# Kernel tuning notes

Measured on AMD Instinct MI355X. Metric: run time of the kernel, lower is better.

## Reference

```python
import jax, jax.numpy as jnp
import numpy as np

B, S, D, H = 8, 2048, 1024, 1024

def setup_inputs() -> dict:
    key = jax.random.key(0)
    ks = jax.random.split(key, 7)
    s = 1.0 / np.sqrt(D)  # torch Linear default init scale (uniform bound)
    x = jax.random.normal(ks[0], (B, S, D), dtype=jnp.float32)
    Wq = jax.random.uniform(ks[1], (D, H), jnp.float32, -s, s)
    bq = jax.random.uniform(ks[2], (H,), jnp.float32, -s, s)
    Wk = jax.random.uniform(ks[3], (D, H), jnp.float32, -s, s)
    bk = jax.random.uniform(ks[4], (H,), jnp.float32, -s, s)
    Wv = jax.random.uniform(ks[5], (D, H), jnp.float32, -s, s)
    bv = jax.random.uniform(ks[6], (H,), jnp.float32, -s, s)
    return {"x": x, "Wq": Wq, "bq": bq, "Wk": Wk, "bk": bk, "Wv": Wv, "bv": bv}

def reference(x, Wq, bq, Wk, bk, Wv, bv):
    scale = jnp.asarray(H ** 0.5, x.dtype)
    q = jnp.einsum('bsd,dh->bsh', x, Wq) + bq
    k = jnp.einsum('bsd,dh->bsh', x, Wk) + bk
    v = jnp.einsum('bsd,dh->bsh', x, Wv) + bv
    scores = jnp.einsum('bqh,bkh->bqk', q, k) / scale  # [B,S,S]
    probs = jax.nn.softmax(scores, axis=-1)
    return jnp.einsum('bqk,bkh->bqh', probs, v)
```

## Files before the change

kernel.cpp:

```cpp
#include <hip/hip_runtime.h>
#include <hip/hip_bf16.h>
#include <stdint.h>

using bf16 = __hip_bfloat16;
typedef __bf16 bf16x8 __attribute__((ext_vector_type(8)));
typedef float f32x4 __attribute__((ext_vector_type(4)));
typedef unsigned short u16x8 __attribute__((ext_vector_type(8)));

#define GLOAD_LDS16(gp, lp)                                                    \
  __builtin_amdgcn_global_load_lds(                                           \
      (const __attribute__((address_space(1))) void*)(gp),                     \
      (__attribute__((address_space(3))) void*)(lp), 16, 0, 0)

#define WAITCNT_VM(N) asm volatile("s_waitcnt vmcnt(" #N ")" ::: "memory")
#define WAITCNT_LGKM0() asm volatile("s_waitcnt lgkmcnt(0)" ::: "memory")

__device__ inline void store_out(bf16* p, float v)  { *p = __float2bfloat16(v); }
__device__ inline void store_out(float* p, float v) { *p = v; }

template <typename OUT_T, int BIAS_AXIS, bool NFAST>
__global__ __launch_bounds__(512, 2) void gemm256(
    const bf16* __restrict__ A, const bf16* __restrict__ Bt,
    const float* __restrict__ bias0, const float* __restrict__ bias1,
    OUT_T* __restrict__ out0, OUT_T* __restrict__ out1, int Nsplit,
    int K, int lda, int ldb, int ldc,
    long long sA, long long sB, long long sC, float alpha)
{
    __shared__ __align__(16) bf16 lds[4 * 16384];

    const int Mt = gridDim.x, Nt = gridDim.y;
    const int nwg = Mt * Nt * gridDim.z;
    const int hw  = blockIdx.x + Mt * (blockIdx.y + Nt * blockIdx.z);
    const int lg  = (nwg & 7) ? hw : ((hw & 7) * (nwg >> 3) + (hw >> 3));
    const int per = Mt * Nt;
    const int zt  = lg / per;
    const int rem = lg - zt * per;
    int mt, nt;
    if (NFAST) { mt = rem / Nt; nt = rem - mt * Nt; }
    else       { mt = rem % Mt; nt = rem / Mt; }

    A  += (long long)zt * sA;
    Bt += (long long)zt * sB;
    out0 += (long long)zt * sC;
    if (out1) out1 += (long long)zt * sC;

    const int bm = mt * 256;
    const int bn = nt * 256;
    const int t = threadIdx.x, lane = t & 63, w = t >> 6;
    const int wm = w >> 2, wn = w & 3;
    const int fr = lane & 15, c16 = lane >> 4;

    const bf16* gsrc[4];
    int lbase[4];
    #pragma unroll
    for (int c = 0; c < 4; ++c) {
        const int idx  = w * 128 + (c & 1) * 64 + lane;
        const int slot = idx & 7;
        const int r    = ((idx >> 3) << 1) | (idx & 1);
        const int cc   = (slot ^ (r & 7)) >> 1;
        if (c < 2) {
            gsrc[c]  = A + (long long)(bm + r) * lda + cc * 8;
            lbase[c] = w * 1024 + c * 512;
        } else {
            gsrc[c]  = Bt + (long long)(bn + r) * ldb + cc * 8;
            lbase[c] = 8192 + w * 1024 + (c - 2) * 512;
        }
    }

    const int sw   = ((fr & 7) ^ (c16 << 1)) * 8;
    const int offA = (wm * 64 + (fr >> 1)) * 64 + sw;
    const int offB = 8192 + (wn * 32 + (fr >> 1)) * 64 + sw;

    const int nk = K >> 5;

    auto STAGE2 = [&](int jt, int h) {
        const int buf = (jt & 3) * 16384;
        GLOAD_LDS16(gsrc[2 * h]     + jt * 32, &lds[buf + lbase[2 * h]]);
        GLOAD_LDS16(gsrc[2 * h + 1] + jt * 32, &lds[buf + lbase[2 * h + 1]]);
    };

    STAGE2(0, 0); STAGE2(0, 1);
    STAGE2(1, 0); STAGE2(1, 1);
    STAGE2(2, 0); STAGE2(2, 1);
    WAITCNT_VM(8);
    __builtin_amdgcn_s_barrier();

    f32x4 acc[8][4] = {};

    for (int j = 0; j < nk; ++j) {
        const int buf = (j & 3) * 16384;
        const bool pref = (j + 3 < nk);

        bf16x8 af[4], bfv[4], af2[4];
        #pragma unroll
        for (int m = 0; m < 4; ++m)
            af[m] = *reinterpret_cast<const bf16x8*>(&lds[buf + offA + m * 512]);
        #pragma unroll
        for (int n = 0; n < 4; ++n)
            bfv[n] = *reinterpret_cast<const bf16x8*>(&lds[buf + offB + n * 512]);
        if (pref) STAGE2(j + 3, 0);

        __builtin_amdgcn_s_barrier();
        WAITCNT_LGKM0();
        __builtin_amdgcn_sched_barrier(0);
        __builtin_amdgcn_s_setprio(1);
        #pragma unroll
        for (int m = 0; m < 4; ++m)
            #pragma unroll
            for (int n = 0; n < 4; ++n)
                acc[m][n] = __builtin_amdgcn_mfma_f32_16x16x32_bf16(
                    af[m], bfv[n], acc[m][n], 0, 0, 0);
        __builtin_amdgcn_s_setprio(0);
        __builtin_amdgcn_sched_barrier(0);
        __builtin_amdgcn_s_barrier();

        #pragma unroll
        for (int m = 0; m < 4; ++m)
            af2[m] = *reinterpret_cast<const bf16x8*>(
                &lds[buf + offA + (m + 4) * 512]);
        if (pref) STAGE2(j + 3, 1);

        __builtin_amdgcn_s_barrier();
        WAITCNT_LGKM0();
        __builtin_amdgcn_sched_barrier(0);
        __builtin_amdgcn_s_setprio(1);
        #pragma unroll
        for (int m = 0; m < 4; ++m)
            #pragma unroll
            for (int n = 0; n < 4; ++n)
                acc[m + 4][n] = __builtin_amdgcn_mfma_f32_16x16x32_bf16(
                    af2[m], bfv[n], acc[m + 4][n], 0, 0, 0);
        __builtin_amdgcn_s_setprio(0);
        __builtin_amdgcn_sched_barrier(0);

        if (j + 3 < nk)      { WAITCNT_VM(8); }
        else if (j + 2 < nk) { WAITCNT_VM(4); }
        else if (j + 1 < nk) { WAITCNT_VM(0); }
        __builtin_amdgcn_s_barrier();
    }

    const int colbase = bn + wn * 64 + fr;
    const int rowbase = bm + wm * 128 + c16 * 4;
    #pragma unroll
    for (int n = 0; n < 4; ++n) {
        const int gc = colbase + n * 16;
        const bool seg0 = gc < Nsplit;
        OUT_T* op = seg0 ? out0 : out1;
        const int col = seg0 ? gc : gc - Nsplit;
        float bcol = 0.0f;
        if (BIAS_AXIS == 0) {
            const float* bp = seg0 ? bias0 : bias1;
            if (bp) bcol = bp[col];
        }
        #pragma unroll
        for (int m = 0; m < 8; ++m) {
            #pragma unroll
            for (int jj = 0; jj < 4; ++jj) {
                const int row = rowbase + m * 16 + jj;
                float v = acc[m][n][jj] * alpha;
                if (BIAS_AXIS == 0) v += bcol;
                else if (bias0)     v += bias0[row];
                store_out(&op[(long long)row * ldc + col], v);
            }
        }
    }
}

__global__ __launch_bounds__(256) void f32_to_bf16(
    const float* __restrict__ in, bf16* __restrict__ out, long long n)
{
    long long i = ((long long)blockIdx.x * 256 + threadIdx.x) * 4;
    const long long stride = (long long)gridDim.x * 256 * 4;
    for (; i < n; i += stride) {
        float4 v = *reinterpret_cast<const float4*>(in + i);
        unsigned ux = __float_as_uint(v.x), uy = __float_as_uint(v.y);
        unsigned uz = __float_as_uint(v.z), uw = __float_as_uint(v.w);
        ushort4 o;
        o.x = (unsigned short)((ux + 0x7fffu + ((ux >> 16) & 1u)) >> 16);
        o.y = (unsigned short)((uy + 0x7fffu + ((uy >> 16) & 1u)) >> 16);
        o.z = (unsigned short)((uz + 0x7fffu + ((uz >> 16) & 1u)) >> 16);
        o.w = (unsigned short)((uw + 0x7fffu + ((uw >> 16) & 1u)) >> 16);
        *reinterpret_cast<ushort4*>(out + i) = o;
    }
}

__global__ void transpose_f32_bf16(const float* __restrict__ in,
                                   bf16* __restrict__ out, int R, int C)
{
    __shared__ float tile[32][33];
    const int c0 = blockIdx.x * 32, r0 = blockIdx.y * 32;
    const int tx = threadIdx.x, ty = threadIdx.y;
    #pragma unroll
    for (int i = ty; i < 32; i += 8)
        tile[i][tx] = in[(long long)(r0 + i) * C + (c0 + tx)];
    __syncthreads();
    #pragma unroll
    for (int i = ty; i < 32; i += 8)
        out[(long long)(c0 + i) * R + (r0 + tx)] = __float2bfloat16(tile[tx][i]);
}

__global__ __launch_bounds__(256) void softmax_rows(bf16* __restrict__ Sbuf, int cols)
{
    __shared__ float red[8];
    bf16* p = Sbuf + (long long)blockIdx.x * cols;
    const int t = threadIdx.x;

    u16x8 v = *reinterpret_cast<const u16x8*>(p + t * 8);
    float f[8];
    #pragma unroll
    for (int i = 0; i < 8; ++i)
        f[i] = __uint_as_float((unsigned)v[i] << 16);

    float m = -3.0e38f;
    #pragma unroll
    for (int i = 0; i < 8; ++i) m = fmaxf(m, f[i]);
    #pragma unroll
    for (int o = 32; o; o >>= 1) m = fmaxf(m, __shfl_xor(m, o));
    if ((t & 63) == 0) red[t >> 6] = m;
    __syncthreads();
    m = fmaxf(fmaxf(red[0], red[1]), fmaxf(red[2], red[3]));

    float s = 0.0f;
    #pragma unroll
    for (int i = 0; i < 8; ++i) { f[i] = __expf(f[i] - m); s += f[i]; }
    #pragma unroll
    for (int o = 32; o; o >>= 1) s += __shfl_xor(s, o);
    __syncthreads();
    if ((t & 63) == 0) red[4 + (t >> 6)] = s;
    __syncthreads();
    s = (red[4] + red[5]) + (red[6] + red[7]);
    const float inv = 1.0f / s;

    u16x8 o16;
    #pragma unroll
    for (int i = 0; i < 8; ++i) {
        unsigned u = __float_as_uint(f[i] * inv);
        o16[i] = (unsigned short)((u + 0x7fffu + ((u >> 16) & 1u)) >> 16);
    }
    *reinterpret_cast<u16x8*>(p + t * 8) = o16;
}

extern "C" void kernel_launch(void* const* d_in, const int* in_sizes, int n_in,
                              void* d_out, int out_size, void* d_ws, size_t ws_size,
                              hipStream_t stream)
{
    const int B = 8, S = 2048, D = 1024, H = 1024;
    const float* x  = (const float*)d_in[0];
    const float* Wq = (const float*)d_in[1];
    const float* bq = (const float*)d_in[2];
    const float* Wk = (const float*)d_in[3];
    const float* bk = (const float*)d_in[4];
    const float* Wv = (const float*)d_in[5];
    const float* bv = (const float*)d_in[6];
    float* out = (float*)d_out;

    const size_t nQKV = (size_t)B * S * H;
    const size_t nW   = (size_t)D * H;
    const long long sSH = (long long)S * H;
    const long long sSS = (long long)S * S;

    dim3 tb(32, 8), g256(256), g512(512);
    const float inv_scale = 1.0f / 32.0f;

    bf16* xb   = (bf16*)d_ws;
    bf16* Q    = xb  + nQKV;
    bf16* Kb   = Q   + nQKV;
    bf16* Vt   = Kb  + nQKV;
    bf16* WtQK = Vt  + nQKV;
    bf16* Wtv  = WtQK + 2 * nW;
    bf16* Sc   = Wtv + nW;

    const size_t tierA = (4 * nQKV + 3 * nW + (size_t)B * S * S) * 2;
    const size_t tierB = (4 * nQKV + 3 * nW + (size_t)S * S) * 2;
    const bool bigA = ws_size >= tierA;
    if (ws_size < tierB) return;

    f32_to_bf16<<<dim3(2048), g256, 0, stream>>>(x, xb, (long long)nQKV);
    transpose_f32_bf16<<<dim3(H / 32, D / 32), tb, 0, stream>>>(Wq, WtQK, D, H);
    transpose_f32_bf16<<<dim3(H / 32, D / 32), tb, 0, stream>>>(Wk, WtQK + nW, D, H);
    transpose_f32_bf16<<<dim3(H / 32, D / 32), tb, 0, stream>>>(Wv, Wtv, D, H);

    gemm256<bf16, 0, true><<<dim3(B * S / 256, 2 * H / 256, 1), g512, 0, stream>>>(
        xb, WtQK, bq, bk, Q, Kb, H, D, D, D, H, 0, 0, 0, 1.0f);

    gemm256<bf16, 1, false><<<dim3(H / 256, B * S / 256, 1), g512, 0, stream>>>(
        Wtv, xb, bv, nullptr, Vt, nullptr, 1 << 30, D, D, D, B * S, 0, 0, 0, 1.0f);

    if (bigA) {
        gemm256<bf16, 0, true><<<dim3(S / 256, S / 256, B), g512, 0, stream>>>(
            Q, Kb, nullptr, nullptr, Sc, nullptr, 1 << 30, H, H, H, S,
            sSH, sSH, sSS, inv_scale);
        softmax_rows<<<dim3(B * S), g256, 0, stream>>>(Sc, S);
        gemm256<float, 0, true><<<dim3(S / 256, H / 256, B), g512, 0, stream>>>(
            Sc, Vt, nullptr, nullptr, out, nullptr, 1 << 30, S, S, B * S, H,
            sSS, (long long)S, sSH, 1.0f);
    } else {
        for (int b = 0; b < B; ++b) {
            gemm256<bf16, 0, true><<<dim3(S / 256, S / 256, 1), g512, 0, stream>>>(
                Q + (size_t)b * sSH, Kb + (size_t)b * sSH, nullptr, nullptr,
                Sc, nullptr, 1 << 30, H, H, H, S, 0, 0, 0, inv_scale);
            softmax_rows<<<dim3(S), g256, 0, stream>>>(Sc, S);
            gemm256<float, 0, true><<<dim3(S / 256, H / 256, 1), g512, 0, stream>>>(
                Sc, Vt + (size_t)b * S, nullptr, nullptr,
                out + (size_t)b * sSH, nullptr, 1 << 30, S, S, B * S, H,
                0, 0, 0, 1.0f);
        }
    }
}
```

Before: 351.6 us.

## Restructure GEMM main loop to K=64 double-buffered quadrant schedule

Rewrites the 256x256 GEMM mainloop so each K-step covers 64 elements instead of 32, with two LDS buffers instead of four. Each K-step is split into four quadrant MFMA phases, and global-to-LDS loads for the next tile are interleaved between them, in the style of a ping-pong schedule. The change aims to raise the MFMA work done per barrier and per LDS read, and to hide load latency better. In exchange it adds more barriers, and it assumes K is a multiple of 128, which risks breaking if K does not divide evenly.

```diff
diff --git a/kernel.cpp b/kernel.cpp
--- a/kernel.cpp
+++ b/kernel.cpp
@@ -12,11 +12,31 @@
       (const __attribute__((address_space(1))) void*)(gp),                     \
       (__attribute__((address_space(3))) void*)(lp), 16, 0, 0)
 
-#define WAITCNT_VM(N) asm volatile("s_waitcnt vmcnt(" #N ")" ::: "memory")
+#define WAITCNT_VM0() asm volatile("s_waitcnt vmcnt(0)" ::: "memory")
+#define WAITCNT_VM2() asm volatile("s_waitcnt vmcnt(2)" ::: "memory")
 #define WAITCNT_LGKM0() asm volatile("s_waitcnt lgkmcnt(0)" ::: "memory")
+#define CFENCE() asm volatile("" ::: "memory")
+#define BAR() do { CFENCE(); __builtin_amdgcn_s_barrier(); CFENCE(); } while (0)
 
 __device__ inline void store_out(bf16* p, float v)  { *p = __float2bfloat16(v); }
 __device__ inline void store_out(float* p, float v) { *p = v; }
+
+template <int QM, int QN>
+__device__ __forceinline__ void mfma_q(f32x4 (&acc)[8][4],
+                                       const bf16x8 (&AV)[4][2],
+                                       const bf16x8 (&BV)[2][2])
+{
+    #pragma unroll
+    for (int kk = 0; kk < 2; ++kk)
+        #pragma unroll
+        for (int mf = 0; mf < 4; ++mf)
+            #pragma unroll
+            for (int nf = 0; nf < 2; ++nf)
+                acc[QM * 4 + mf][QN * 2 + nf] =
+                    __builtin_amdgcn_mfma_f32_16x16x32_bf16(
+                        AV[mf][kk], BV[nf][kk],
+                        acc[QM * 4 + mf][QN * 2 + nf], 0, 0, 0);
+}
 
 template <typename OUT_T, int BIAS_AXIS, bool NFAST>
 __global__ __launch_bounds__(512, 2) void gemm256(
@@ -26,7 +46,7 @@
     int K, int lda, int ldb, int ldc,
     long long sA, long long sB, long long sC, float alpha)
 {
-    __shared__ __align__(16) bf16 lds[4 * 16384];
+    __shared__ __align__(16) bf16 lds[65536];
 
     const int Mt = gridDim.x, Nt = gridDim.y;
     const int nwg = Mt * Nt * gridDim.z;
@@ -35,108 +55,120 @@
     const int per = Mt * Nt;
     const int zt  = lg / per;
     const int rem = lg - zt * per;
-    int mt, nt;
-    if (NFAST) { mt = rem / Nt; nt = rem - mt * Nt; }
-    else       { mt = rem % Mt; nt = rem / Mt; }
+    int mt, ntile;
+    if (NFAST) { mt = rem / Nt; ntile = rem - mt * Nt; }
+    else       { mt = rem % Mt; ntile = rem / Mt; }
 
     A  += (long long)zt * sA;
     Bt += (long long)zt * sB;
     out0 += (long long)zt * sC;
     if (out1) out1 += (long long)zt * sC;
 
-    const int bm = mt * 256;
-    const int bn = nt * 256;
-    const int t = threadIdx.x, lane = t & 63, w = t >> 6;
-    const int wm = w >> 2, wn = w & 3;
+    const int bm = mt * 256, bn = ntile * 256;
+    const int t = threadIdx.x, lane = t & 63;
+    const int w = t >> 6, wm = w >> 2, wn = w & 3;
     const int fr = lane & 15, c16 = lane >> 4;
 
-    const bf16* gsrc[4];
-    int lbase[4];
-    #pragma unroll
-    for (int c = 0; c < 4; ++c) {
-        const int idx  = w * 128 + (c & 1) * 64 + lane;
-        const int slot = idx & 7;
-        const int r    = ((idx >> 3) << 1) | (idx & 1);
-        const int cc   = (slot ^ (r & 7)) >> 1;
-        if (c < 2) {
-            gsrc[c]  = A + (long long)(bm + r) * lda + cc * 8;
-            lbase[c] = w * 1024 + c * 512;
-        } else {
-            gsrc[c]  = Bt + (long long)(bn + r) * ldb + cc * 8;
-            lbase[c] = 8192 + w * 1024 + (c - 2) * 512;
-        }
-    }
-
-    const int sw   = ((fr & 7) ^ (c16 << 1)) * 8;
-    const int offA = (wm * 64 + (fr >> 1)) * 64 + sw;
-    const int offB = 8192 + (wn * 32 + (fr >> 1)) * 64 + sw;
-
-    const int nk = K >> 5;
-
-    auto STAGE2 = [&](int jt, int h) {
-        const int buf = (jt & 3) * 16384;
-        GLOAD_LDS16(gsrc[2 * h]     + jt * 32, &lds[buf + lbase[2 * h]]);
-        GLOAD_LDS16(gsrc[2 * h + 1] + jt * 32, &lds[buf + lbase[2 * h + 1]]);
-    };
-
-    STAGE2(0, 0); STAGE2(0, 1);
-    STAGE2(1, 0); STAGE2(1, 1);
-    STAGE2(2, 0); STAGE2(2, 1);
-    WAITCNT_VM(8);
-    __builtin_amdgcn_s_barrier();
+    const int sr  = t >> 3;
+    const int scc = ((t & 7) ^ (sr & 7)) << 3;
+    const bf16* pA = A  + (long long)(bm + sr) * lda + scc;
+    const bf16* pB = Bt + (long long)(bn + sr) * ldb + scc;
+    const int ldst = t * 8;
+
+#define STAGE_A(HALF, JT, BUFO) do {                                           \
+    const bf16* _s = pA + (long long)(HALF) * 128 * lda + (JT) * 64;           \
+    GLOAD_LDS16(_s, &lds[(BUFO) + (HALF) * 8192 + ldst]);                      \
+    GLOAD_LDS16(_s + 64 * (long long)lda,                                      \
+                &lds[(BUFO) + (HALF) * 8192 + ldst + 4096]);                   \
+} while (0)
+#define STAGE_B(HALF, JT, BUFO) do {                                           \
+    const bf16* _s = pB + (long long)(HALF) * 128 * ldb + (JT) * 64;           \
+    GLOAD_LDS16(_s, &lds[(BUFO) + 16384 + (HALF) * 8192 + ldst]);              \
+    GLOAD_LDS16(_s + 64 * (long long)ldb,                                      \
+                &lds[(BUFO) + 16384 + (HALF) * 8192 + ldst + 4096]);           \
+} while (0)
+
+    const int axor0 = ((c16    ) ^ (fr & 7)) << 3;
+    const int axor1 = ((c16 + 4) ^ (fr & 7)) << 3;
+    const int aoffc = wm * 8192 + fr * 64;
+    const int boffc = 16384 + (wn * 64 + fr) * 64;
+
+#define RD(e) (*reinterpret_cast<const bf16x8*>(&lds[(e)]))
+#define READ_A(QM, BUFO) do {                                                  \
+    _Pragma("unroll") for (int mf = 0; mf < 4; ++mf) {                         \
+        aA[mf][0] = RD((BUFO) + aoffc + (QM) * 4096 + mf * 1024 + axor0);      \
+        aA[mf][1] = RD((BUFO) + aoffc + (QM) * 4096 + mf * 1024 + axor1);      \
+    } } while (0)
+#define READ_B(QN, BV, BUFO) do {                                              \
+    _Pragma("unroll") for (int nf = 0; nf < 2; ++nf) {                         \
+        BV[nf][0] = RD((BUFO) + boffc + (QN) * 2048 + nf * 1024 + axor0);      \
+        BV[nf][1] = RD((BUFO) + boffc + (QN) * 2048 + nf * 1024 + axor1);      \
+    } } while (0)
+
+    const int nk = K >> 6;
+    const int niter = nk >> 1;
 
     f32x4 acc[8][4] = {};
-
-    for (int j = 0; j < nk; ++j) {
-        const int buf = (j & 3) * 16384;
-        const bool pref = (j + 3 < nk);
-
-        bf16x8 af[4], bfv[4], af2[4];
-        #pragma unroll
-        for (int m = 0; m < 4; ++m)
-            af[m] = *reinterpret_cast<const bf16x8*>(&lds[buf + offA + m * 512]);
-        #pragma unroll
-        for (int n = 0; n < 4; ++n)
-            bfv[n] = *reinterpret_cast<const bf16x8*>(&lds[buf + offB + n * 512]);
-        if (pref) STAGE2(j + 3, 0);
-
-        __builtin_amdgcn_s_barrier();
-        WAITCNT_LGKM0();
-        __builtin_amdgcn_sched_barrier(0);
-        __builtin_amdgcn_s_setprio(1);
-        #pragma unroll
-        for (int m = 0; m < 4; ++m)
-            #pragma unroll
-            for (int n = 0; n < 4; ++n)
-                acc[m][n] = __builtin_amdgcn_mfma_f32_16x16x32_bf16(
-                    af[m], bfv[n], acc[m][n], 0, 0, 0);
+    bf16x8 aA[4][2], bQ0[2][2], bQ1[2][2];
+
+    STAGE_A(0, 0, 0); STAGE_A(1, 0, 0); STAGE_B(0, 0, 0); STAGE_B(1, 0, 0);
+    STAGE_A(0, 1, 32768);
+    WAITCNT_VM2();
+    BAR();
+
+    for (int it = 0; it < niter; ++it) {
+        const int t2 = it * 2;
+        const bool tail = (it == niter - 1);
+
+        READ_A(0, 0); READ_B(0, bQ0, 0);
+        STAGE_A(1, t2 + 1, 32768);
+        BAR(); WAITCNT_LGKM0(); __builtin_amdgcn_sched_barrier(0);
+        __builtin_amdgcn_s_setprio(1); mfma_q<0, 0>(acc, aA, bQ0);
+        __builtin_amdgcn_s_setprio(0); BAR();
+
+        READ_B(1, bQ1, 0);
+        STAGE_B(0, t2 + 1, 32768);
+        BAR(); WAITCNT_LGKM0(); __builtin_amdgcn_sched_barrier(0);
+        __builtin_amdgcn_s_setprio(1); mfma_q<0, 1>(acc, aA, bQ1);
+        __builtin_amdgcn_s_setprio(0); BAR();
+
+        READ_A(1, 0);
+        STAGE_B(1, t2 + 1, 32768);
+        BAR(); WAITCNT_LGKM0(); __builtin_amdgcn_sched_barrier(0);
+        __builtin_amdgcn_s_setprio(1); mfma_q<1, 1>(acc, aA, bQ1);
+        __builtin_amdgcn_s_setprio(0); BAR();
+
+        if (!tail) STAGE_A(0, t2 + 2, 0);
+        BAR();
+        __builtin_amdgcn_s_setprio(1); mfma_q<1, 0>(acc, aA, bQ0);
         __builtin_amdgcn_s_setprio(0);
-        __builtin_amdgcn_sched_barrier(0);
-        __builtin_amdgcn_s_barrier();
-
-        #pragma unroll
-        for (int m = 0; m < 4; ++m)
-            af2[m] = *reinterpret_cast<const bf16x8*>(
-                &lds[buf + offA + (m + 4) * 512]);
-        if (pref) STAGE2(j + 3, 1);
-
-        __builtin_amdgcn_s_barrier();
-        WAITCNT_LGKM0();
-        __builtin_amdgcn_sched_barrier(0);
-        __builtin_amdgcn_s_setprio(1);
-        #pragma unroll
-        for (int m = 0; m < 4; ++m)
-            #pragma unroll
-            for (int n = 0; n < 4; ++n)
-                acc[m + 4][n] = __builtin_amdgcn_mfma_f32_16x16x32_bf16(
-                    af2[m], bfv[n], acc[m + 4][n], 0, 0, 0);
+        if (tail) { WAITCNT_VM0(); } else { WAITCNT_VM2(); }
+        BAR();
+
+        READ_A(0, 32768); READ_B(0, bQ0, 32768);
+        if (!tail) STAGE_A(1, t2 + 2, 0);
+        BAR(); WAITCNT_LGKM0(); __builtin_amdgcn_sched_barrier(0);
+        __builtin_amdgcn_s_setprio(1); mfma_q<0, 0>(acc, aA, bQ0);
+        __builtin_amdgcn_s_setprio(0); BAR();
+
+        READ_B(1, bQ1, 32768);
+        if (!tail) STAGE_B(0, t2 + 2, 0);
+        BAR(); WAITCNT_LGKM0(); __builtin_amdgcn_sched_barrier(0);
+        __builtin_amdgcn_s_setprio(1); mfma_q<0, 1>(acc, aA, bQ1);
+        __builtin_amdgcn_s_setprio(0); BAR();
+
+        READ_A(1, 32768);
+        if (!tail) STAGE_B(1, t2 + 2, 0);
+        BAR(); WAITCNT_LGKM0(); __builtin_amdgcn_sched_barrier(0);
+        __builtin_amdgcn_s_setprio(1); mfma_q<1, 1>(acc, aA, bQ1);
+        __builtin_amdgcn_s_setprio(0); BAR();
+
+        if (!tail) STAGE_A(0, t2 + 3, 32768);
+        BAR();
+        __builtin_amdgcn_s_setprio(1); mfma_q<1, 0>(acc, aA, bQ0);
         __builtin_amdgcn_s_setprio(0);
-        __builtin_amdgcn_sched_barrier(0);
-
-        if (j + 3 < nk)      { WAITCNT_VM(8); }
-        else if (j + 2 < nk) { WAITCNT_VM(4); }
-        else if (j + 1 < nk) { WAITCNT_VM(0); }
-        __builtin_amdgcn_s_barrier();
+        if (!tail) WAITCNT_VM2();
+        BAR();
     }
 
     const int colbase = bn + wn * 64 + fr;
@@ -164,6 +196,11 @@
             }
         }
     }
+#undef STAGE_A
+#undef STAGE_B
+#undef RD
+#undef READ_A
+#undef READ_B
 }
 
 __global__ __launch_bounds__(256) void f32_to_bf16(
```

Measured after the change: 328.2 us. 6.7% less time.
